# Optimization experiments

Hardware: AMD Instinct MI355X
Metric: run time of the kernel (lower is better)

Reference implementation:

```python
import jax, jax.numpy as jnp
import numpy as np

B, C, H, W = 16384, 1, 2048, 1
HID = 5


def setup_inputs() -> dict:
    key = jax.random.key(0)
    kx, kl, k1, k2, k3, k4 = jax.random.split(key, 6)
    x = jax.random.normal(kx, (B, C, H, W), dtype=jnp.float32)
    # random ragged lengths in [1, H]; zero out padded tail so the module's
    # (x != 0).any(dim=2) mask recovers exactly these lengths
    lengths = jax.random.randint(kl, (B,), 1, H + 1)
    t_idx = jnp.arange(H)
    valid = (t_idx[None, :] < lengths[:, None])  # [B, H]
    x = x * valid[:, None, :, None].astype(jnp.float32)
    s = 1.0 / np.sqrt(HID)
    W_ih = jax.random.uniform(k1, (4 * HID, 1), minval=-s, maxval=s, dtype=jnp.float32)
    W_hh = jax.random.uniform(k2, (4 * HID, HID), minval=-s, maxval=s, dtype=jnp.float32)
    b_ih = jax.random.uniform(k3, (4 * HID,), minval=-s, maxval=s, dtype=jnp.float32)
    b_hh = jax.random.uniform(k4, (4 * HID,), minval=-s, maxval=s, dtype=jnp.float32)
    return {"x": x, "W_ih": W_ih, "W_hh": W_hh, "b_ih": b_ih, "b_hh": b_hh}


def reference(x, W_ih, W_hh, b_ih, b_hh):
    b, c, h, w = x.shape
    feats = c * w  # == 1 (LSTM input_size)
    xr = x.reshape(b, h, feats)  # [B, T, 1]
    mask = jnp.any(xr != 0, axis=2)  # [B, T]
    lengths = mask.sum(axis=1).astype(jnp.int32)  # [B]

    bias = b_ih + b_hh  # [4H]
    # precompute input projection for all timesteps: [B, T, 4H]
    x_proj = jnp.einsum('btf,gf->btg', xr, W_ih) + bias
    xs = jnp.moveaxis(x_proj, 1, 0)  # [T, B, 4H]

    h0 = jnp.zeros((b, HID), dtype=x.dtype)
    c0 = jnp.zeros((b, HID), dtype=x.dtype)

    def step(carry, inp):
        hp, cp = carry
        xg, t = inp
        gates = xg + hp @ W_hh.T  # [B, 4H]
        i, f, g, o = jnp.split(gates, 4, axis=1)
        i = jax.nn.sigmoid(i)
        f = jax.nn.sigmoid(f)
        g = jnp.tanh(g)
        o = jax.nn.sigmoid(o)
        cn = f * cp + i * g
        hn = o * jnp.tanh(cn)
        # packed semantics: only advance state while t < length (per sample)
        upd = (t < lengths)[:, None]
        hn = jnp.where(upd, hn, hp)
        cn = jnp.where(upd, cn, cp)
        return (hn, cn), None

    (hT, cT), _ = jax.lax.scan(step, (h0, c0), (xs, jnp.arange(h)))
    return hT[None]  # [1, B, HID] matching torch h shape
```

## Files before the change

kernel.cpp:

```cpp
#include <hip/hip_runtime.h>

#define Bn    16384
#define Tn    2048
#define HIDn  5
#define NBINS 2048

typedef float v2f __attribute__((ext_vector_type(2)));

static __device__ __forceinline__ float rcp_fast(float v) {
    return __builtin_amdgcn_rcpf(v);
}
static __device__ __forceinline__ float med3(float x, float lo, float hi) {
    return __builtin_amdgcn_fmed3f(x, lo, hi);
}

template <int K>
static __device__ __forceinline__ float bcast8(float v) {
    return __int_as_float(
        __builtin_amdgcn_ds_swizzle(__float_as_int(v), (K << 5) | 0x18));
}

__global__ void zero_kernel(int* __restrict__ gbins) {
    gbins[blockIdx.x * 256 + threadIdx.x] = 0;
}

__global__ __launch_bounds__(256) void len_kernel(const float* __restrict__ x,
                                                  int* __restrict__ lengths,
                                                  int* __restrict__ gbins) {
    const int gtid = blockIdx.x * 256 + threadIdx.x;
    const int row  = gtid >> 6;
    const int lane = threadIdx.x & 63;
    const float4* r = reinterpret_cast<const float4*>(x + (size_t)row * Tn);
    int cnt = 0;
    #pragma unroll
    for (int i = 0; i < Tn / 4 / 64; ++i) {
        float4 v = r[i * 64 + lane];
        cnt += (v.x != 0.0f) + (v.y != 0.0f) + (v.z != 0.0f) + (v.w != 0.0f);
    }
    #pragma unroll
    for (int off = 32; off > 0; off >>= 1) cnt += __shfl_xor(cnt, off, 64);
    if (lane == 0) {
        lengths[row] = cnt;
        const int d = max(0, min(NBINS - 1, NBINS - cnt));
        atomicAdd(&gbins[d], 1);
    }
}

__global__ __launch_bounds__(1024) void sort_kernel(const int* __restrict__ lengths,
                                                    const int* __restrict__ gbins,
                                                    int* __restrict__ perm) {
    __shared__ int bins[NBINS];
    __shared__ int bsum[1024];
    const int tid = threadIdx.x;
    bins[tid]        = gbins[tid];
    bins[tid + 1024] = gbins[tid + 1024];
    __syncthreads();
    const int a0 = bins[2 * tid], a1 = bins[2 * tid + 1];
    const int s = a0 + a1;
    bsum[tid] = s;
    __syncthreads();
    int acc = s;
    for (int off = 1; off < 1024; off <<= 1) {
        int v = (tid >= off) ? bsum[tid - off] : 0;
        __syncthreads();
        acc += v;
        bsum[tid] = acc;
        __syncthreads();
    }
    const int excl = acc - s;
    bins[2 * tid]     = excl;
    bins[2 * tid + 1] = excl + a0;
    __syncthreads();
    for (int i = tid; i < Bn; i += 1024) {
        int d = NBINS - lengths[i];
        d = max(0, min(NBINS - 1, d));
        const int p = atomicAdd(&bins[d], 1);
        perm[p] = i;
    }
}

__global__ __launch_bounds__(256, 2) void lstm_kernel(const float* __restrict__ x,
                                                      const float* __restrict__ Wih,
                                                      const float* __restrict__ Whh,
                                                      const float* __restrict__ bih,
                                                      const float* __restrict__ bhh,
                                                      const int* __restrict__ lengths,
                                                      const int* __restrict__ perm,
                                                      float* __restrict__ out) {
    const int gtid = blockIdx.x * 256 + threadIdx.x;
    const int grp  = gtid >> 3;
    const int lsub = threadIdx.x & 7;
    const int k    = min(lsub, 4);

    const int b   = perm[grp];
    const int len = lengths[b];

    v2f wihA, wihB, bA, bB, whhA[HIDn], whhB[HIDn];
    {
        const int gi = k, gf = 5 + k, gg = 10 + k, go = 15 + k;
        wihA = (v2f){ Wih[gi] * 0.5f, Wih[gf] * 0.5f };
        wihB = (v2f){ Wih[gg],        Wih[go] * 0.5f };
        bA   = (v2f){ (bih[gi] + bhh[gi]) * 0.5f, (bih[gf] + bhh[gf]) * 0.5f };
        bB   = (v2f){ (bih[gg] + bhh[gg]),        (bih[go] + bhh[go]) * 0.5f };
        #pragma unroll
        for (int kk = 0; kk < HIDn; ++kk) {
            whhA[kk] = (v2f){ Whh[gi * HIDn + kk] * 0.5f, Whh[gf * HIDn + kk] * 0.5f };
            whhB[kk] = (v2f){ Whh[gg * HIDn + kk],        Whh[go * HIDn + kk] * 0.5f };
        }
    }

    const float* xrow = x + (size_t)b * Tn;
    float h0 = 0, h1 = 0, h2 = 0, h3 = 0, h4 = 0;
    float hq = 0, c = 0;

    float4 xq = *reinterpret_cast<const float4*>(xrow);
    for (int t = 0; __any(t < len); t += 4) {
        const float4 xn = *reinterpret_cast<const float4*>(xrow + min(t + 4, Tn - 4));
        const float xs[4] = { xq.x, xq.y, xq.z, xq.w };
        #pragma unroll
        for (int s = 0; s < 4; ++s) {
            const float xv = xs[s];
            v2f pA = xv * wihA + bA;
            v2f pB = xv * wihB + bB;
            pA = h0 * whhA[0] + pA;  pB = h0 * whhB[0] + pB;
            pA = h1 * whhA[1] + pA;  pB = h1 * whhB[1] + pB;
            pA = h2 * whhA[2] + pA;  pB = h2 * whhB[2] + pB;
            pA = h3 * whhA[3] + pA;  pB = h3 * whhB[3] + pB;
            pA = h4 * whhA[4] + pA;  pB = h4 * whhB[4] + pB;
            v2f tA, tB;
            tA.x = med3(pA.x, -4.0f, 4.0f);  tA.y = med3(pA.y, -4.0f, 4.0f);
            tB.x = med3(pB.x, -4.0f, 4.0f);  tB.y = med3(pB.y, -4.0f, 4.0f);
            const v2f zA = tA * tA, zB = tB * tB;
            const v2f nA = (zA * 21.0f + 1260.0f) * zA + 10395.0f;
            const v2f nB = (zB * 21.0f + 1260.0f) * zB + 10395.0f;
            const v2f dA = ((zA + 210.0f) * zA + 4725.0f) * zA + 10395.0f;
            const v2f dB = ((zB + 210.0f) * zB + 4725.0f) * zB + 10395.0f;
            const float rA = rcp_fast(dA.x * dA.y);
            const float rB = rcp_fast(dB.x * dB.y);
            const v2f pnA = tA * nA, pnB = tB * nB;
            const float ti = (pnA.x * dA.y) * rA;
            const float tf = (pnA.y * dA.x) * rA;
            const float tg = (pnB.x * dB.y) * rB;
            const float to = (pnB.y * dB.x) * rB;
            const float gi_ = fmaf(ti, 0.5f, 0.5f);
            const float gf_ = fmaf(tf, 0.5f, 0.5f);
            const float oo  = fmaf(to, 0.5f, 0.5f);

            const float cn = fmaf(gf_, c, gi_ * tg);

            const float tc = med3(cn, -4.0f, 4.0f);
            const float zc = tc * tc;
            const float nc = fmaf(zc, fmaf(zc, 21.0f, 1260.0f), 10395.0f);
            const float dc = fmaf(zc, fmaf(zc, zc + 210.0f, 4725.0f), 10395.0f);
            const float hn = (tc * nc) * (oo * rcp_fast(dc));

            const bool upd = (t + s) < len;
            c  = upd ? cn : c;
            hq = upd ? hn : hq;

            h0 = bcast8<0>(hq);
            h1 = bcast8<1>(hq);
            h2 = bcast8<2>(hq);
            h3 = bcast8<3>(hq);
            h4 = bcast8<4>(hq);
        }
        xq = xn;
    }

    if (lsub < HIDn) out[(size_t)b * HIDn + lsub] = hq;
}

extern "C" void kernel_launch(void* const* d_in, const int* in_sizes, int n_in,
                              void* d_out, int out_size, void* d_ws, size_t ws_size,
                              hipStream_t stream) {
    const float* x   = (const float*)d_in[0];
    const float* Wih = (const float*)d_in[1];
    const float* Whh = (const float*)d_in[2];
    const float* bih = (const float*)d_in[3];
    const float* bhh = (const float*)d_in[4];
    float* out = (float*)d_out;

    int* lengths = (int*)d_ws;
    int* perm    = lengths + Bn;
    int* gbins   = perm + Bn;

    zero_kernel<<<NBINS / 256, 256, 0, stream>>>(gbins);
    len_kernel<<<Bn / 4, 256, 0, stream>>>(x, lengths, gbins);
    sort_kernel<<<1, 1024, 0, stream>>>(lengths, gbins, perm);
    lstm_kernel<<<Bn * 8 / 256, 256, 0, stream>>>(x, Wih, Whh, bih, bhh,
                                                  lengths, perm, out);
}
```

Before: 573.0 us.

## Map each LSTM sample to four lanes with DPP quad broadcasts

Each sample now uses a quad of four lanes instead of eight. Each lane computes its own hidden unit, and the fifth unit's four gates are spread across the quad and gathered with DPP quad_perm broadcasts, which replace the ds_swizzle exchange. Lanes no longer idle in groups of eight, so the grid halves and the per-lane work per step grows. The time loop is also unrolled to 8 steps, and the recurrent dot products are split into two partial sums to shorten the dependency chain. This adds per-step ALU work and register pressure, and the occupancy hint on launch bounds is removed.

```diff
diff --git a/kernel.cpp b/kernel.cpp
--- a/kernel.cpp
+++ b/kernel.cpp
@@ -14,10 +14,11 @@
     return __builtin_amdgcn_fmed3f(x, lo, hi);
 }
 
-template <int K>
-static __device__ __forceinline__ float bcast8(float v) {
+template <int SRC>
+static __device__ __forceinline__ float qbcast(float v) {
+    constexpr int ctrl = SRC | (SRC << 2) | (SRC << 4) | (SRC << 6);
     return __int_as_float(
-        __builtin_amdgcn_ds_swizzle(__float_as_int(v), (K << 5) | 0x18));
+        __builtin_amdgcn_update_dpp(0, __float_as_int(v), ctrl, 0xF, 0xF, true));
 }
 
 __global__ void zero_kernel(int* __restrict__ gbins) {
@@ -79,95 +80,135 @@
     }
 }
 
-__global__ __launch_bounds__(256, 2) void lstm_kernel(const float* __restrict__ x,
-                                                      const float* __restrict__ Wih,
-                                                      const float* __restrict__ Whh,
-                                                      const float* __restrict__ bih,
-                                                      const float* __restrict__ bhh,
-                                                      const int* __restrict__ lengths,
-                                                      const int* __restrict__ perm,
-                                                      float* __restrict__ out) {
+__global__ __launch_bounds__(256) void lstm_kernel(const float* __restrict__ x,
+                                                   const float* __restrict__ Wih,
+                                                   const float* __restrict__ Whh,
+                                                   const float* __restrict__ bih,
+                                                   const float* __restrict__ bhh,
+                                                   const int* __restrict__ lengths,
+                                                   const int* __restrict__ perm,
+                                                   float* __restrict__ out) {
     const int gtid = blockIdx.x * 256 + threadIdx.x;
-    const int grp  = gtid >> 3;
-    const int lsub = threadIdx.x & 7;
-    const int k    = min(lsub, 4);
+    const int grp  = gtid >> 2;
+    const int q    = gtid & 3;
 
     const int b   = perm[grp];
     const int len = lengths[b];
 
-    v2f wihA, wihB, bA, bB, whhA[HIDn], whhB[HIDn];
+    v2f wihA, wihB, bsA, bsB, whhA[HIDn], whhB[HIDn];
+    float wih4, bs4, whh4[HIDn];
     {
-        const int gi = k, gf = 5 + k, gg = 10 + k, go = 15 + k;
+        const int gi = q, gf = 5 + q, gg = 10 + q, go = 15 + q, g4 = 5 * q + 4;
+        const float s4 = (q == 2) ? 1.0f : 0.5f;
         wihA = (v2f){ Wih[gi] * 0.5f, Wih[gf] * 0.5f };
         wihB = (v2f){ Wih[gg],        Wih[go] * 0.5f };
-        bA   = (v2f){ (bih[gi] + bhh[gi]) * 0.5f, (bih[gf] + bhh[gf]) * 0.5f };
-        bB   = (v2f){ (bih[gg] + bhh[gg]),        (bih[go] + bhh[go]) * 0.5f };
+        wih4 = Wih[g4] * s4;
+        bsA  = (v2f){ (bih[gi] + bhh[gi]) * 0.5f, (bih[gf] + bhh[gf]) * 0.5f };
+        bsB  = (v2f){ (bih[gg] + bhh[gg]),        (bih[go] + bhh[go]) * 0.5f };
+        bs4  = (bih[g4] + bhh[g4]) * s4;
         #pragma unroll
         for (int kk = 0; kk < HIDn; ++kk) {
             whhA[kk] = (v2f){ Whh[gi * HIDn + kk] * 0.5f, Whh[gf * HIDn + kk] * 0.5f };
             whhB[kk] = (v2f){ Whh[gg * HIDn + kk],        Whh[go * HIDn + kk] * 0.5f };
+            whh4[kk] = Whh[g4 * HIDn + kk] * s4;
         }
     }
+    const float m4 = (q == 2) ? 1.0f : 0.5f;
+    const float a4b = (q == 2) ? 0.0f : 0.5f;
 
     const float* xrow = x + (size_t)b * Tn;
     float h0 = 0, h1 = 0, h2 = 0, h3 = 0, h4 = 0;
-    float hq = 0, c = 0;
-
-    float4 xq = *reinterpret_cast<const float4*>(xrow);
-    for (int t = 0; __any(t < len); t += 4) {
-        const float4 xn = *reinterpret_cast<const float4*>(xrow + min(t + 4, Tn - 4));
-        const float xs[4] = { xq.x, xq.y, xq.z, xq.w };
+    float hq = 0, cq = 0, c4 = 0;
+
+    float4 xA = *reinterpret_cast<const float4*>(xrow);
+    float4 xB = *reinterpret_cast<const float4*>(xrow + 4);
+    for (int t = 0; __any(t < len); t += 8) {
+        const float4 nA = *reinterpret_cast<const float4*>(xrow + min(t + 8,  Tn - 8));
+        const float4 nB = *reinterpret_cast<const float4*>(xrow + min(t + 12, Tn - 4));
+        const float xs[8] = { xA.x, xA.y, xA.z, xA.w, xB.x, xB.y, xB.z, xB.w };
+
         #pragma unroll
-        for (int s = 0; s < 4; ++s) {
+        for (int s = 0; s < 8; ++s) {
             const float xv = xs[s];
-            v2f pA = xv * wihA + bA;
-            v2f pB = xv * wihB + bB;
-            pA = h0 * whhA[0] + pA;  pB = h0 * whhB[0] + pB;
-            pA = h1 * whhA[1] + pA;  pB = h1 * whhB[1] + pB;
-            pA = h2 * whhA[2] + pA;  pB = h2 * whhB[2] + pB;
-            pA = h3 * whhA[3] + pA;  pB = h3 * whhB[3] + pB;
-            pA = h4 * whhA[4] + pA;  pB = h4 * whhB[4] + pB;
+            v2f   pA = xv * wihA + bsA;
+            v2f   pB = xv * wihB + bsB;
+            float p4 = fmaf(xv, wih4, bs4);
+            v2f uA = h0 * whhA[0] + pA;
+            v2f uB = h0 * whhB[0] + pB;
+            uA = h1 * whhA[1] + uA;   uB = h1 * whhB[1] + uB;
+            uA = h2 * whhA[2] + uA;   uB = h2 * whhB[2] + uB;
+            v2f vA = h4 * whhA[4] + h3 * whhA[3];
+            v2f vB = h4 * whhB[4] + h3 * whhB[3];
+            pA = uA + vA;  pB = uB + vB;
+            {
+                float u4 = fmaf(h0, whh4[0], p4);
+                u4 = fmaf(h1, whh4[1], u4);
+                u4 = fmaf(h2, whh4[2], u4);
+                float v4 = fmaf(h4, whh4[4], h3 * whh4[3]);
+                p4 = u4 + v4;
+            }
             v2f tA, tB;
             tA.x = med3(pA.x, -4.0f, 4.0f);  tA.y = med3(pA.y, -4.0f, 4.0f);
             tB.x = med3(pB.x, -4.0f, 4.0f);  tB.y = med3(pB.y, -4.0f, 4.0f);
+            const float t4c = med3(p4, -4.0f, 4.0f);
             const v2f zA = tA * tA, zB = tB * tB;
-            const v2f nA = (zA * 21.0f + 1260.0f) * zA + 10395.0f;
-            const v2f nB = (zB * 21.0f + 1260.0f) * zB + 10395.0f;
+            const float z4 = t4c * t4c;
+            const v2f nAp = (zA * 21.0f + 1260.0f) * zA + 10395.0f;
+            const v2f nBp = (zB * 21.0f + 1260.0f) * zB + 10395.0f;
+            const float n4 = fmaf(z4, fmaf(z4, 21.0f, 1260.0f), 10395.0f);
             const v2f dA = ((zA + 210.0f) * zA + 4725.0f) * zA + 10395.0f;
             const v2f dB = ((zB + 210.0f) * zB + 4725.0f) * zB + 10395.0f;
+            const float d4 = fmaf(z4, fmaf(z4, z4 + 210.0f, 4725.0f), 10395.0f);
             const float rA = rcp_fast(dA.x * dA.y);
             const float rB = rcp_fast(dB.x * dB.y);
-            const v2f pnA = tA * nA, pnB = tB * nB;
-            const float ti = (pnA.x * dA.y) * rA;
-            const float tf = (pnA.y * dA.x) * rA;
-            const float tg = (pnB.x * dB.y) * rB;
-            const float to = (pnB.y * dB.x) * rB;
+            const float r4 = rcp_fast(d4);
+            const v2f pnA = tA * nAp, pnB = tB * nBp;
+            const float ti = pnA.x * (dA.y * rA);
+            const float tf = pnA.y * (dA.x * rA);
+            const float tg = pnB.x * (dB.y * rB);
+            const float to = pnB.y * (dB.x * rB);
+            const float t4v = (t4c * n4) * r4;
             const float gi_ = fmaf(ti, 0.5f, 0.5f);
             const float gf_ = fmaf(tf, 0.5f, 0.5f);
-            const float oo  = fmaf(to, 0.5f, 0.5f);
-
-            const float cn = fmaf(gf_, c, gi_ * tg);
-
-            const float tc = med3(cn, -4.0f, 4.0f);
-            const float zc = tc * tc;
-            const float nc = fmaf(zc, fmaf(zc, 21.0f, 1260.0f), 10395.0f);
-            const float dc = fmaf(zc, fmaf(zc, zc + 210.0f, 4725.0f), 10395.0f);
-            const float hn = (tc * nc) * (oo * rcp_fast(dc));
+            const float go_ = fmaf(to, 0.5f, 0.5f);
+            const float a4  = fmaf(t4v, m4, a4b);
+
+            const float cnq = fmaf(gf_, cq, gi_ * tg);
+
+            const float i4 = qbcast<0>(a4);
+            const float f4 = qbcast<1>(a4);
+            const float g4v = qbcast<2>(a4);
+            const float o4 = qbcast<3>(a4);
+            const float cn4 = fmaf(f4, c4, i4 * g4v);
+
+            v2f tC;
+            tC.x = med3(cnq, -4.0f, 4.0f);
+            tC.y = med3(cn4, -4.0f, 4.0f);
+            const v2f zC = tC * tC;
+            const v2f nC = (zC * 21.0f + 1260.0f) * zC + 10395.0f;
+            const v2f dC = ((zC + 210.0f) * zC + 4725.0f) * zC + 10395.0f;
+            const float rC = rcp_fast(dC.x * dC.y);
+            const v2f pnC = tC * nC;
+            const float hnq = (pnC.x * (dC.y * rC)) * go_;
+            const float hn4 = (pnC.y * (dC.x * rC)) * o4;
 
             const bool upd = (t + s) < len;
-            c  = upd ? cn : c;
-            hq = upd ? hn : hq;
-
-            h0 = bcast8<0>(hq);
-            h1 = bcast8<1>(hq);
-            h2 = bcast8<2>(hq);
-            h3 = bcast8<3>(hq);
-            h4 = bcast8<4>(hq);
+            cq = upd ? cnq : cq;
+            c4 = upd ? cn4 : c4;
+            hq = upd ? hnq : hq;
+            h4 = upd ? hn4 : h4;
+
+            h0 = qbcast<0>(hq);
+            h1 = qbcast<1>(hq);
+            h2 = qbcast<2>(hq);
+            h3 = qbcast<3>(hq);
         }
-        xq = xn;
-    }
-
-    if (lsub < HIDn) out[(size_t)b * HIDn + lsub] = hq;
+        xA = nA;
+        xB = nB;
+    }
+
+    out[(size_t)b * HIDn + q] = hq;
+    if (q == 0) out[(size_t)b * HIDn + 4] = h4;
 }
 
 extern "C" void kernel_launch(void* const* d_in, const int* in_sizes, int n_in,
@@ -187,6 +228,6 @@
     zero_kernel<<<NBINS / 256, 256, 0, stream>>>(gbins);
     len_kernel<<<Bn / 4, 256, 0, stream>>>(x, lengths, gbins);
     sort_kernel<<<1, 1024, 0, stream>>>(lengths, gbins, perm);
-    lstm_kernel<<<Bn * 8 / 256, 256, 0, stream>>>(x, Wih, Whh, bih, bhh,
+    lstm_kernel<<<Bn * 4 / 256, 256, 0, stream>>>(x, Wih, Whh, bih, bhh,
                                                   lengths, perm, out);
 }
```

Result: slower. 623.0 us (+8.7%).
